# Performance work log

Measured on AMD Instinct MI355X. Metric: run time of the kernel, lower is better.

Reference implementation:

```python
import jax, jax.numpy as jnp
import numpy as np

N = 262144        # 64^3 grid unknowns
NNZ = 7 * N       # ~7-point stencil sparsity
BS = 32


def setup_inputs() -> dict:
    key = jax.random.key(0)
    k1, k2, k3, k4, k5 = jax.random.split(key, 5)
    y_pred = jax.random.normal(k1, (BS, N), dtype=jnp.float32)
    y_true = jax.random.normal(k2, (BS, N), dtype=jnp.float32)
    A_vals = jax.random.normal(k3, (NNZ,), dtype=jnp.float32)
    A_rows = jax.random.randint(k4, (NNZ,), 0, N, dtype=jnp.int32)
    A_cols = jax.random.randint(k5, (NNZ,), 0, N, dtype=jnp.int32)
    return {"y_pred": y_pred, "y_true": y_true, "A_vals": A_vals,
            "A_rows": A_rows, "A_cols": A_cols}


def reference(y_pred, y_true, A_vals, A_rows, A_cols):
    # YhatY[b] = <y_true[b], y_pred[b]>
    YhatY = jnp.sum(y_true * y_pred, axis=1)                      # (bs,)
    # Sparse matvec per batch: YhatAt = (A @ y_pred.T).T, COO form.
    # gathered[e, b] = A_vals[e] * y_pred[b, A_cols[e]]
    gathered = (y_pred[:, A_cols] * A_vals).T                     # (nnz, bs)
    YhatAt = jax.ops.segment_sum(gathered, A_rows, num_segments=N).T  # (bs, N)
    # YhatYhatAt[b] = <y_pred[b], A y_pred[b]>
    YhatYhatAt = jnp.sum(y_pred * YhatAt, axis=1)                 # (bs,)
    # diag(YhatY / YhatYhatAt) @ YhatAt == row-wise scale by alpha
    alpha = YhatY / YhatYhatAt                                    # (bs,)
    resid = y_true - alpha[:, None] * YhatAt                      # (bs, N)
    return jnp.mean(jnp.sum(resid * resid, axis=1))
```

## Files before the change

kernel.cpp:

```cpp
#include <hip/hip_runtime.h>

#define NGRID 262144
#define NNZ_C 1835008
#define TP    260


__global__ __launch_bounds__(256) void k_prep(
        const float* __restrict__ yp, const float* __restrict__ yt,
        float* __restrict__ yp_t, float* __restrict__ yt_t,
        float* __restrict__ yat_t) {
    __shared__ __align__(16) float T[32 * TP];
    const int tid = threadIdx.x;
    const int l = tid & 63, w = tid >> 6;
    const int fam = blockIdx.x >> 10;
    const size_t n0 = (size_t)(blockIdx.x & 1023) * 256;
    const float* src = fam ? yt : yp;
    #pragma unroll
    for (int s = 0; s < 8; ++s) {
        const int b = s * 4 + w;
        const float4 a = *(const float4*)(src + (size_t)b * NGRID + n0 + 4 * l);
        *(float4*)(&T[b * TP + 4 * l]) = a;
    }
    __syncthreads();
    float4* dst4 = (float4*)((fam ? yt_t : yp_t) + n0 * 32);
    float4* yat4 = (float4*)(yat_t + n0 * 32);
    #pragma unroll
    for (int q = 0; q < 8; ++q) {
        const int f = q * 256 + tid;
        const int n = f >> 3;
        const int bb = 4 * (f & 7);
        float4 v;
        v.x = T[(bb + 0) * TP + n];
        v.y = T[(bb + 1) * TP + n];
        v.z = T[(bb + 2) * TP + n];
        v.w = T[(bb + 3) * TP + n];
        dst4[f] = v;
        if (!fam) yat4[f] = make_float4(0.f, 0.f, 0.f, 0.f);
    }
}

__global__ void k_scatter(const float* __restrict__ vals,
                          const int* __restrict__ rows,
                          const int* __restrict__ cols,
                          const float* __restrict__ yp_t,
                          float* __restrict__ yat_t) {
    const size_t tid = (size_t)blockIdx.x * blockDim.x + threadIdx.x;
    const int b = (int)(tid & 31);
    const size_t e = tid >> 5;
    const float v = vals[e];
    const int r = rows[e];
    const int c = cols[e];
    const float x = yp_t[(size_t)c * 32 + b];
    atomicAdd(&yat_t[(size_t)r * 32 + b], v * x);
}

__global__ __launch_bounds__(256) void k_post(
        const float* __restrict__ yat_t, const float* __restrict__ yp_t,
        const float* __restrict__ yt_t, float* __restrict__ p2) {
    __shared__ float redA[5][1024];
    const int tid = threadIdx.x;
    const size_t base = (size_t)blockIdx.x * 1024;
    const float4* yat4 = (const float4*)yat_t;
    const float4* yp4 = (const float4*)yp_t;
    const float4* yt4 = (const float4*)yt_t;
    float c1[4] = {0,0,0,0}, c2[4] = {0,0,0,0}, c3[4] = {0,0,0,0};
    float tt[4] = {0,0,0,0}, sy[4] = {0,0,0,0};
    #pragma unroll
    for (int q = 0; q < 4; ++q) {
        const size_t f = base + q * 256 + tid;
        const float4 a = yat4[f];
        const float4 p = yp4[f];
        const float4 t = yt4[f];
        c1[0] = fmaf(p.x, a.x, c1[0]); c2[0] = fmaf(t.x, a.x, c2[0]);
        c3[0] = fmaf(a.x, a.x, c3[0]); tt[0] = fmaf(t.x, t.x, tt[0]);
        sy[0] = fmaf(t.x, p.x, sy[0]);
        c1[1] = fmaf(p.y, a.y, c1[1]); c2[1] = fmaf(t.y, a.y, c2[1]);
        c3[1] = fmaf(a.y, a.y, c3[1]); tt[1] = fmaf(t.y, t.y, tt[1]);
        sy[1] = fmaf(t.y, p.y, sy[1]);
        c1[2] = fmaf(p.z, a.z, c1[2]); c2[2] = fmaf(t.z, a.z, c2[2]);
        c3[2] = fmaf(a.z, a.z, c3[2]); tt[2] = fmaf(t.z, t.z, tt[2]);
        sy[2] = fmaf(t.z, p.z, sy[2]);
        c1[3] = fmaf(p.w, a.w, c1[3]); c2[3] = fmaf(t.w, a.w, c2[3]);
        c3[3] = fmaf(a.w, a.w, c3[3]); tt[3] = fmaf(t.w, t.w, tt[3]);
        sy[3] = fmaf(t.w, p.w, sy[3]);
    }
    #pragma unroll
    for (int k = 0; k < 4; ++k) {
        redA[0][4 * tid + k] = c1[k];
        redA[1][4 * tid + k] = c2[k];
        redA[2][4 * tid + k] = c3[k];
        redA[3][4 * tid + k] = tt[k];
        redA[4][4 * tid + k] = sy[k];
    }
    __syncthreads();
    if (tid < 32) {
        #pragma unroll
        for (int s = 0; s < 5; ++s) {
            float acc = 0.f;
            #pragma unroll
            for (int j = 0; j < 32; ++j) acc += redA[s][tid + 32 * j];
            p2[blockIdx.x * 160 + s * 32 + tid] = acc;
        }
    }
}

__global__ __launch_bounds__(256) void k_finish1(
        const float* __restrict__ p2, float* __restrict__ pr2) {
    const int tid = threadIdx.x, g = blockIdx.x;
    if (tid < 160) {
        float acc = 0.f;
        #pragma unroll
        for (int j = 0; j < 32; ++j) acc += p2[(size_t)(g * 32 + j) * 160 + tid];
        pr2[g * 160 + tid] = acc;
    }
}

__global__ __launch_bounds__(256) void k_finish2(
        const float* __restrict__ pr2, float* __restrict__ out) {
    __shared__ float tot[160];
    __shared__ float lb[32];
    const int tid = threadIdx.x;
    if (tid < 160) {
        float acc = 0.f;
        #pragma unroll
        for (int j = 0; j < 64; ++j) acc += pr2[j * 160 + tid];
        tot[tid] = acc;
    }
    __syncthreads();
    if (tid < 32) {
        const float c1 = tot[0 + tid];
        const float c2 = tot[32 + tid];
        const float c3 = tot[64 + tid];
        const float stt = tot[96 + tid];
        const float sty = tot[128 + tid];
        const float a = sty / c1;
        lb[tid] = fmaf(a * a, c3, fmaf(-2.f * a, c2, stt));
    }
    __syncthreads();
    if (tid == 0) {
        float s = 0.f;
        #pragma unroll
        for (int i = 0; i < 32; ++i) s += lb[i];
        out[0] = s * (1.0f / 32.0f);
    }
}

extern "C" void kernel_launch(void* const* d_in, const int* in_sizes, int n_in,
                              void* d_out, int out_size, void* d_ws, size_t ws_size,
                              hipStream_t stream) {
    const float* yp = (const float*)d_in[0];
    const float* yt = (const float*)d_in[1];
    const float* Av = (const float*)d_in[2];
    const int*   Ar = (const int*)d_in[3];
    const int*   Ac = (const int*)d_in[4];
    float* out = (float*)d_out;

    float* ws    = (float*)d_ws;
    float* yp_t  = ws;
    float* yat_t = yp_t + (size_t)NGRID * 32;
    float* yt_t  = yat_t + (size_t)NGRID * 32;
    float* p2    = yt_t + (size_t)NGRID * 32;
    float* pr2   = p2 + 2048 * 160;

    k_prep<<<2048, 256, 0, stream>>>(yp, yt, yp_t, yt_t, yat_t);
    k_scatter<<<(NNZ_C * 32) / 256, 256, 0, stream>>>(Av, Ar, Ac, yp_t, yat_t);
    k_post<<<2048, 256, 0, stream>>>(yat_t, yp_t, yt_t, p2);
    k_finish1<<<64, 256, 0, stream>>>(p2, pr2);
    k_finish2<<<1, 256, 0, stream>>>(pr2, out);
}
```

Measured before the change: 339.0 us.

## Bucket COO entries by row block and accumulate SpMM in shared memory

Replaces the global-atomic COO scatter with a counting-sort pass: a histogram of row blocks of 128, a scan, and a bucketing pass that packs column, local row and value into uint2. A per-bucket kernel then gathers yp_t, accumulates into shared-memory atomics, and fuses the post-reduction dot products, so the yat_t buffer, its zeroing and its separate read-back are gone. This removes about 58M global float atomics and a full intermediate write and read. In exchange it adds three extra kernels, global atomics per nonzero for the histogram and cursor, and a non-deterministic bucket order.

```diff
diff --git a/kernel.cpp b/kernel.cpp
--- a/kernel.cpp
+++ b/kernel.cpp
@@ -3,14 +3,19 @@
 #define NGRID 262144
 #define NNZ_C 1835008
 #define TP    260
+#define NBKT  2048
 
 
 __global__ __launch_bounds__(256) void k_prep(
         const float* __restrict__ yp, const float* __restrict__ yt,
         float* __restrict__ yp_t, float* __restrict__ yt_t,
-        float* __restrict__ yat_t) {
+        unsigned* __restrict__ counts) {
     __shared__ __align__(16) float T[32 * TP];
     const int tid = threadIdx.x;
+    if (blockIdx.x == 0) {
+        #pragma unroll
+        for (int i = 0; i < 8; ++i) counts[i * 256 + tid] = 0u;
+    }
     const int l = tid & 63, w = tid >> 6;
     const int fam = blockIdx.x >> 10;
     const size_t n0 = (size_t)(blockIdx.x & 1023) * 256;
@@ -23,7 +28,6 @@
     }
     __syncthreads();
     float4* dst4 = (float4*)((fam ? yt_t : yp_t) + n0 * 32);
-    float4* yat4 = (float4*)(yat_t + n0 * 32);
     #pragma unroll
     for (int q = 0; q < 8; ++q) {
         const int f = q * 256 + tid;
@@ -35,71 +39,120 @@
         v.z = T[(bb + 2) * TP + n];
         v.w = T[(bb + 3) * TP + n];
         dst4[f] = v;
-        if (!fam) yat4[f] = make_float4(0.f, 0.f, 0.f, 0.f);
-    }
-}
-
-__global__ void k_scatter(const float* __restrict__ vals,
-                          const int* __restrict__ rows,
-                          const int* __restrict__ cols,
-                          const float* __restrict__ yp_t,
-                          float* __restrict__ yat_t) {
-    const size_t tid = (size_t)blockIdx.x * blockDim.x + threadIdx.x;
-    const int b = (int)(tid & 31);
-    const size_t e = tid >> 5;
+    }
+}
+
+__global__ __launch_bounds__(256) void k_hist(const int* __restrict__ rows,
+                                              unsigned* __restrict__ counts) {
+    const size_t i4 = (size_t)blockIdx.x * 256 + threadIdx.x;
+    const int4 r = ((const int4*)rows)[i4];
+    atomicAdd(&counts[(unsigned)r.x >> 7], 1u);
+    atomicAdd(&counts[(unsigned)r.y >> 7], 1u);
+    atomicAdd(&counts[(unsigned)r.z >> 7], 1u);
+    atomicAdd(&counts[(unsigned)r.w >> 7], 1u);
+}
+
+__global__ __launch_bounds__(256) void k_scan(
+        const unsigned* __restrict__ counts,
+        unsigned* __restrict__ offs, unsigned* __restrict__ cursor) {
+    __shared__ unsigned ts[256];
+    const int tid = threadIdx.x;
+    unsigned c[8];
+    unsigned s = 0;
+    #pragma unroll
+    for (int i = 0; i < 8; ++i) { c[i] = counts[tid * 8 + i]; s += c[i]; }
+    ts[tid] = s;
+    __syncthreads();
+    for (int d = 1; d < 256; d <<= 1) {
+        const unsigned v = (tid >= d) ? ts[tid - d] : 0u;
+        __syncthreads();
+        ts[tid] += v;
+        __syncthreads();
+    }
+    unsigned base = (tid == 0) ? 0u : ts[tid - 1];
+    #pragma unroll
+    for (int i = 0; i < 8; ++i) {
+        offs[tid * 8 + i] = base;
+        cursor[tid * 8 + i] = base;
+        base += c[i];
+    }
+}
+
+__global__ __launch_bounds__(256) void k_bucket(
+        const float* __restrict__ vals, const int* __restrict__ rows,
+        const int* __restrict__ cols, unsigned* __restrict__ cursor,
+        uint2* __restrict__ bkt) {
+    const size_t e = (size_t)blockIdx.x * 256 + threadIdx.x;
+    const unsigned r = (unsigned)rows[e];
+    const unsigned c = (unsigned)cols[e];
     const float v = vals[e];
-    const int r = rows[e];
-    const int c = cols[e];
-    const float x = yp_t[(size_t)c * 32 + b];
-    atomicAdd(&yat_t[(size_t)r * 32 + b], v * x);
-}
-
-__global__ __launch_bounds__(256) void k_post(
-        const float* __restrict__ yat_t, const float* __restrict__ yp_t,
-        const float* __restrict__ yt_t, float* __restrict__ p2) {
-    __shared__ float redA[5][1024];
-    const int tid = threadIdx.x;
-    const size_t base = (size_t)blockIdx.x * 1024;
-    const float4* yat4 = (const float4*)yat_t;
-    const float4* yp4 = (const float4*)yp_t;
-    const float4* yt4 = (const float4*)yt_t;
-    float c1[4] = {0,0,0,0}, c2[4] = {0,0,0,0}, c3[4] = {0,0,0,0};
-    float tt[4] = {0,0,0,0}, sy[4] = {0,0,0,0};
-    #pragma unroll
-    for (int q = 0; q < 4; ++q) {
-        const size_t f = base + q * 256 + tid;
-        const float4 a = yat4[f];
-        const float4 p = yp4[f];
-        const float4 t = yt4[f];
-        c1[0] = fmaf(p.x, a.x, c1[0]); c2[0] = fmaf(t.x, a.x, c2[0]);
-        c3[0] = fmaf(a.x, a.x, c3[0]); tt[0] = fmaf(t.x, t.x, tt[0]);
-        sy[0] = fmaf(t.x, p.x, sy[0]);
-        c1[1] = fmaf(p.y, a.y, c1[1]); c2[1] = fmaf(t.y, a.y, c2[1]);
-        c3[1] = fmaf(a.y, a.y, c3[1]); tt[1] = fmaf(t.y, t.y, tt[1]);
-        sy[1] = fmaf(t.y, p.y, sy[1]);
-        c1[2] = fmaf(p.z, a.z, c1[2]); c2[2] = fmaf(t.z, a.z, c2[2]);
-        c3[2] = fmaf(a.z, a.z, c3[2]); tt[2] = fmaf(t.z, t.z, tt[2]);
-        sy[2] = fmaf(t.z, p.z, sy[2]);
-        c1[3] = fmaf(p.w, a.w, c1[3]); c2[3] = fmaf(t.w, a.w, c2[3]);
-        c3[3] = fmaf(a.w, a.w, c3[3]); tt[3] = fmaf(t.w, t.w, tt[3]);
-        sy[3] = fmaf(t.w, p.w, sy[3]);
-    }
-    #pragma unroll
-    for (int k = 0; k < 4; ++k) {
-        redA[0][4 * tid + k] = c1[k];
-        redA[1][4 * tid + k] = c2[k];
-        redA[2][4 * tid + k] = c3[k];
-        redA[3][4 * tid + k] = tt[k];
-        redA[4][4 * tid + k] = sy[k];
-    }
+    const unsigned pos = atomicAdd(&cursor[r >> 7], 1u);
+    bkt[pos] = make_uint2(c | ((r & 127u) << 18), __float_as_uint(v));
+}
+
+__global__ __launch_bounds__(256) void k_accum(
+        const uint2* __restrict__ bkt, const unsigned* __restrict__ offs,
+        const unsigned* __restrict__ counts,
+        const float* __restrict__ yp_t, const float* __restrict__ yt_t,
+        float* __restrict__ p2) {
+    __shared__ float acc[128 * 32];
+    const int tid = threadIdx.x;
+    const int g = blockIdx.x;
+    #pragma unroll
+    for (int i = 0; i < 16; ++i) acc[i * 256 + tid] = 0.f;
+    __syncthreads();
+    const unsigned base = offs[g];
+    const unsigned cnt = counts[g];
+    const int b = tid & 31;
+    const uint2* eb = bkt + base;
+    unsigned i = (unsigned)(tid >> 5);
+    for (; i + 24 < cnt; i += 32) {
+        const uint2 e0 = eb[i];
+        const uint2 e1 = eb[i + 8];
+        const uint2 e2 = eb[i + 16];
+        const uint2 e3 = eb[i + 24];
+        const float x0 = yp_t[(size_t)(e0.x & 0x3FFFFu) * 32 + b];
+        const float x1 = yp_t[(size_t)(e1.x & 0x3FFFFu) * 32 + b];
+        const float x2 = yp_t[(size_t)(e2.x & 0x3FFFFu) * 32 + b];
+        const float x3 = yp_t[(size_t)(e3.x & 0x3FFFFu) * 32 + b];
+        atomicAdd(&acc[(e0.x >> 18) * 32 + b], __uint_as_float(e0.y) * x0);
+        atomicAdd(&acc[(e1.x >> 18) * 32 + b], __uint_as_float(e1.y) * x1);
+        atomicAdd(&acc[(e2.x >> 18) * 32 + b], __uint_as_float(e2.y) * x2);
+        atomicAdd(&acc[(e3.x >> 18) * 32 + b], __uint_as_float(e3.y) * x3);
+    }
+    for (; i < cnt; i += 8) {
+        const uint2 e = eb[i];
+        const float x = yp_t[(size_t)(e.x & 0x3FFFFu) * 32 + b];
+        atomicAdd(&acc[(e.x >> 18) * 32 + b], __uint_as_float(e.y) * x);
+    }
+    __syncthreads();
+    float c1 = 0.f, c2 = 0.f, c3 = 0.f, st = 0.f, sy = 0.f;
+    const float* ypg = yp_t + (size_t)g * 4096;
+    const float* ytg = yt_t + (size_t)g * 4096;
+    #pragma unroll
+    for (int q = 0; q < 16; ++q) {
+        const int idx = q * 256 + tid;
+        const float a = acc[idx];
+        const float p = ypg[idx];
+        const float t = ytg[idx];
+        c1 = fmaf(p, a, c1); c2 = fmaf(t, a, c2); c3 = fmaf(a, a, c3);
+        st = fmaf(t, t, st); sy = fmaf(t, p, sy);
+    }
+    __syncthreads();
+    float* red = acc;
+    red[0 * 256 + tid] = c1;
+    red[1 * 256 + tid] = c2;
+    red[2 * 256 + tid] = c3;
+    red[3 * 256 + tid] = st;
+    red[4 * 256 + tid] = sy;
     __syncthreads();
     if (tid < 32) {
         #pragma unroll
         for (int s = 0; s < 5; ++s) {
-            float acc = 0.f;
+            float a2 = 0.f;
             #pragma unroll
-            for (int j = 0; j < 32; ++j) acc += redA[s][tid + 32 * j];
-            p2[blockIdx.x * 160 + s * 32 + tid] = acc;
+            for (int j = 0; j < 8; ++j) a2 += red[s * 256 + tid + 32 * j];
+            p2[(size_t)g * 160 + s * 32 + tid] = a2;
         }
     }
 }
@@ -155,16 +208,21 @@
     const int*   Ac = (const int*)d_in[4];
     float* out = (float*)d_out;
 
-    float* ws    = (float*)d_ws;
-    float* yp_t  = ws;
-    float* yat_t = yp_t + (size_t)NGRID * 32;
-    float* yt_t  = yat_t + (size_t)NGRID * 32;
-    float* p2    = yt_t + (size_t)NGRID * 32;
-    float* pr2   = p2 + 2048 * 160;
-
-    k_prep<<<2048, 256, 0, stream>>>(yp, yt, yp_t, yt_t, yat_t);
-    k_scatter<<<(NNZ_C * 32) / 256, 256, 0, stream>>>(Av, Ar, Ac, yp_t, yat_t);
-    k_post<<<2048, 256, 0, stream>>>(yat_t, yp_t, yt_t, p2);
+    float*    ws     = (float*)d_ws;
+    float*    yp_t   = ws;
+    float*    yt_t   = yp_t + (size_t)NGRID * 32;
+    uint2*    bkt    = (uint2*)(yt_t + (size_t)NGRID * 32);
+    unsigned* counts = (unsigned*)(bkt + NNZ_C);
+    unsigned* offs   = counts + NBKT;
+    unsigned* cursor = offs + NBKT;
+    float*    p2     = (float*)(cursor + NBKT);
+    float*    pr2    = p2 + 2048 * 160;
+
+    k_prep<<<2048, 256, 0, stream>>>(yp, yt, yp_t, yt_t, counts);
+    k_hist<<<NNZ_C / 1024, 256, 0, stream>>>(Ar, counts);
+    k_scan<<<1, 256, 0, stream>>>(counts, offs, cursor);
+    k_bucket<<<NNZ_C / 256, 256, 0, stream>>>(Av, Ar, Ac, cursor, bkt);
+    k_accum<<<NBKT, 256, 0, stream>>>(bkt, offs, counts, yp_t, yt_t, p2);
     k_finish1<<<64, 256, 0, stream>>>(p2, pr2);
     k_finish2<<<1, 256, 0, stream>>>(pr2, out);
 }
```

Measured after the change: 874.0 us. 2.58x slower.

## Skip transposing y_true; read original layouts in post kernel via shared-memory transpose

Applied to the files above, without the earlier changes.

The prep kernel no longer transposes y_true into a batch-interleaved buffer. The post kernel instead transposes its tile of yat back into shared memory and reads y_pred and y_true directly in their original row-major layout. This removes one full 32 MB write plus a later read of the transposed y_true, and shrinks the reduction grids accordingly. It adds shared-memory transpose work and shuffle-based reductions in the post kernel.

```diff
diff --git a/kernel.cpp b/kernel.cpp
--- a/kernel.cpp
+++ b/kernel.cpp
@@ -3,26 +3,25 @@
 #define NGRID 262144
 #define NNZ_C 1835008
 #define TP    260
+#define NS    256
+#define TPAD  260
 
 
 __global__ __launch_bounds__(256) void k_prep(
-        const float* __restrict__ yp, const float* __restrict__ yt,
-        float* __restrict__ yp_t, float* __restrict__ yt_t,
+        const float* __restrict__ yp, float* __restrict__ yp_t,
         float* __restrict__ yat_t) {
     __shared__ __align__(16) float T[32 * TP];
     const int tid = threadIdx.x;
     const int l = tid & 63, w = tid >> 6;
-    const int fam = blockIdx.x >> 10;
-    const size_t n0 = (size_t)(blockIdx.x & 1023) * 256;
-    const float* src = fam ? yt : yp;
+    const size_t n0 = (size_t)blockIdx.x * 256;
     #pragma unroll
     for (int s = 0; s < 8; ++s) {
         const int b = s * 4 + w;
-        const float4 a = *(const float4*)(src + (size_t)b * NGRID + n0 + 4 * l);
+        const float4 a = *(const float4*)(yp + (size_t)b * NGRID + n0 + 4 * l);
         *(float4*)(&T[b * TP + 4 * l]) = a;
     }
     __syncthreads();
-    float4* dst4 = (float4*)((fam ? yt_t : yp_t) + n0 * 32);
+    float4* dst4 = (float4*)(yp_t + n0 * 32);
     float4* yat4 = (float4*)(yat_t + n0 * 32);
     #pragma unroll
     for (int q = 0; q < 8; ++q) {
@@ -35,7 +34,7 @@
         v.z = T[(bb + 2) * TP + n];
         v.w = T[(bb + 3) * TP + n];
         dst4[f] = v;
-        if (!fam) yat4[f] = make_float4(0.f, 0.f, 0.f, 0.f);
+        yat4[f] = make_float4(0.f, 0.f, 0.f, 0.f);
     }
 }
 
@@ -55,52 +54,64 @@
 }
 
 __global__ __launch_bounds__(256) void k_post(
-        const float* __restrict__ yat_t, const float* __restrict__ yp_t,
-        const float* __restrict__ yt_t, float* __restrict__ p2) {
-    __shared__ float redA[5][1024];
+        const float* __restrict__ yat_t, const float* __restrict__ yp,
+        const float* __restrict__ yt, float* __restrict__ p2) {
+    __shared__ __align__(16) float T[32 * TPAD];
     const int tid = threadIdx.x;
-    const size_t base = (size_t)blockIdx.x * 1024;
-    const float4* yat4 = (const float4*)yat_t;
-    const float4* yp4 = (const float4*)yp_t;
-    const float4* yt4 = (const float4*)yt_t;
-    float c1[4] = {0,0,0,0}, c2[4] = {0,0,0,0}, c3[4] = {0,0,0,0};
-    float tt[4] = {0,0,0,0}, sy[4] = {0,0,0,0};
+    const int g = blockIdx.x;
+    const size_t n0 = (size_t)g * NS;
+    const float4* yat4 = (const float4*)(yat_t + n0 * 32);
     #pragma unroll
-    for (int q = 0; q < 4; ++q) {
-        const size_t f = base + q * 256 + tid;
-        const float4 a = yat4[f];
-        const float4 p = yp4[f];
-        const float4 t = yt4[f];
-        c1[0] = fmaf(p.x, a.x, c1[0]); c2[0] = fmaf(t.x, a.x, c2[0]);
-        c3[0] = fmaf(a.x, a.x, c3[0]); tt[0] = fmaf(t.x, t.x, tt[0]);
-        sy[0] = fmaf(t.x, p.x, sy[0]);
-        c1[1] = fmaf(p.y, a.y, c1[1]); c2[1] = fmaf(t.y, a.y, c2[1]);
-        c3[1] = fmaf(a.y, a.y, c3[1]); tt[1] = fmaf(t.y, t.y, tt[1]);
-        sy[1] = fmaf(t.y, p.y, sy[1]);
-        c1[2] = fmaf(p.z, a.z, c1[2]); c2[2] = fmaf(t.z, a.z, c2[2]);
-        c3[2] = fmaf(a.z, a.z, c3[2]); tt[2] = fmaf(t.z, t.z, tt[2]);
-        sy[2] = fmaf(t.z, p.z, sy[2]);
-        c1[3] = fmaf(p.w, a.w, c1[3]); c2[3] = fmaf(t.w, a.w, c2[3]);
-        c3[3] = fmaf(a.w, a.w, c3[3]); tt[3] = fmaf(t.w, t.w, tt[3]);
-        sy[3] = fmaf(t.w, p.w, sy[3]);
+    for (int q = 0; q < 8; ++q) {
+        const int f = q * 256 + tid;
+        const int n = f >> 3;
+        const int b0 = 4 * (f & 7);
+        const float4 v = yat4[f];
+        T[(b0 + 0) * TPAD + n] = v.x;
+        T[(b0 + 1) * TPAD + n] = v.y;
+        T[(b0 + 2) * TPAD + n] = v.z;
+        T[(b0 + 3) * TPAD + n] = v.w;
+    }
+    __syncthreads();
+    const int b = tid >> 3, j = tid & 7;
+    const float* ytb = yt + (size_t)b * NGRID + n0;
+    const float* ypb = yp + (size_t)b * NGRID + n0;
+    const float* Tb = &T[b * TPAD];
+    float c1 = 0.f, c2 = 0.f, c3 = 0.f, st = 0.f, sy = 0.f;
+    #pragma unroll
+    for (int s = 0; s < NS / 32; ++s) {
+        const int n = 4 * j + 32 * s;
+        const float4 a = *(const float4*)(Tb + n);
+        const float4 t = *(const float4*)(ytb + n);
+        const float4 p = *(const float4*)(ypb + n);
+        c1 = fmaf(p.x, a.x, c1); c2 = fmaf(t.x, a.x, c2);
+        c3 = fmaf(a.x, a.x, c3); st = fmaf(t.x, t.x, st);
+        sy = fmaf(t.x, p.x, sy);
+        c1 = fmaf(p.y, a.y, c1); c2 = fmaf(t.y, a.y, c2);
+        c3 = fmaf(a.y, a.y, c3); st = fmaf(t.y, t.y, st);
+        sy = fmaf(t.y, p.y, sy);
+        c1 = fmaf(p.z, a.z, c1); c2 = fmaf(t.z, a.z, c2);
+        c3 = fmaf(a.z, a.z, c3); st = fmaf(t.z, t.z, st);
+        sy = fmaf(t.z, p.z, sy);
+        c1 = fmaf(p.w, a.w, c1); c2 = fmaf(t.w, a.w, c2);
+        c3 = fmaf(a.w, a.w, c3); st = fmaf(t.w, t.w, st);
+        sy = fmaf(t.w, p.w, sy);
     }
     #pragma unroll
-    for (int k = 0; k < 4; ++k) {
-        redA[0][4 * tid + k] = c1[k];
-        redA[1][4 * tid + k] = c2[k];
-        redA[2][4 * tid + k] = c3[k];
-        redA[3][4 * tid + k] = tt[k];
-        redA[4][4 * tid + k] = sy[k];
+    for (int d = 4; d; d >>= 1) {
+        c1 += __shfl_down(c1, d, 8);
+        c2 += __shfl_down(c2, d, 8);
+        c3 += __shfl_down(c3, d, 8);
+        st += __shfl_down(st, d, 8);
+        sy += __shfl_down(sy, d, 8);
     }
-    __syncthreads();
-    if (tid < 32) {
-        #pragma unroll
-        for (int s = 0; s < 5; ++s) {
-            float acc = 0.f;
-            #pragma unroll
-            for (int j = 0; j < 32; ++j) acc += redA[s][tid + 32 * j];
-            p2[blockIdx.x * 160 + s * 32 + tid] = acc;
-        }
+    if (j == 0) {
+        float* row = p2 + (size_t)g * 160;
+        row[0 * 32 + b] = c1;
+        row[1 * 32 + b] = c2;
+        row[2 * 32 + b] = c3;
+        row[3 * 32 + b] = st;
+        row[4 * 32 + b] = sy;
     }
 }
 
@@ -123,7 +134,7 @@
     if (tid < 160) {
         float acc = 0.f;
         #pragma unroll
-        for (int j = 0; j < 64; ++j) acc += pr2[j * 160 + tid];
+        for (int j = 0; j < 32; ++j) acc += pr2[j * 160 + tid];
         tot[tid] = acc;
     }
     __syncthreads();
@@ -158,13 +169,12 @@
     float* ws    = (float*)d_ws;
     float* yp_t  = ws;
     float* yat_t = yp_t + (size_t)NGRID * 32;
-    float* yt_t  = yat_t + (size_t)NGRID * 32;
-    float* p2    = yt_t + (size_t)NGRID * 32;
-    float* pr2   = p2 + 2048 * 160;
+    float* p2    = yat_t + (size_t)NGRID * 32;
+    float* pr2   = p2 + 1024 * 160;
 
-    k_prep<<<2048, 256, 0, stream>>>(yp, yt, yp_t, yt_t, yat_t);
+    k_prep<<<1024, 256, 0, stream>>>(yp, yp_t, yat_t);
     k_scatter<<<(NNZ_C * 32) / 256, 256, 0, stream>>>(Av, Ar, Ac, yp_t, yat_t);
-    k_post<<<2048, 256, 0, stream>>>(yat_t, yp_t, yt_t, p2);
-    k_finish1<<<64, 256, 0, stream>>>(p2, pr2);
+    k_post<<<1024, 256, 0, stream>>>(yat_t, yp, yt, p2);
+    k_finish1<<<32, 256, 0, stream>>>(p2, pr2);
     k_finish2<<<1, 256, 0, stream>>>(pr2, out);
 }
```

Measured after the change: 323.4 us. -4.6%, faster.
